# Kernel optimization log

Measured on AMD Instinct MI355X. Metric: run time of the kernel, lower is better.

The kernel has to match this reference:

```python
import jax, jax.numpy as jnp
import numpy as np


def setup_inputs() -> dict:
    key = jax.random.key(0)
    kx, ky = jax.random.split(key)
    N, D = 8192, 128
    x = jax.random.normal(kx, (N, D), dtype=jnp.float32)
    y = jax.random.normal(ky, (N, D), dtype=jnp.float32)
    return {"x": x, "y": y}


def reference(x, y):
    # L2 contrastive loss (Kostic et al. 2024, NCP):
    #   1/(N(N-1)) * sum_{i != j} <x_i, y_j>^2  -  2/N * sum_i <x_i, y_i>
    N = x.shape[0]
    K = x @ y.T                      # (N, N) pairwise dot products
    diag = jnp.diagonal(K)           # <x_i, y_i>
    off_diag_sq = jnp.sum(K * K) - jnp.sum(diag * diag)
    loss = off_diag_sq / (N * (N - 1)) - 2.0 / N * jnp.sum(diag)
    return loss
```

## Files before the change

### kernel.cpp

```cpp
#include <hip/hip_runtime.h>

#define DD 128
#define SR 72

typedef float f32x4 __attribute__((ext_vector_type(4)));
typedef short s16x8 __attribute__((ext_vector_type(8)));

__global__ __launch_bounds__(512)
void gram_kernel(const float* __restrict__ x, const float* __restrict__ y,
                 float* __restrict__ apart, float* __restrict__ bpart,
                 double* __restrict__ sc, int N, int P)
{
  const int blk = blockIdx.x;
  const bool isX = blk < P;
  const int p = isX ? blk : blk - P;
  const float* __restrict__ src = isX ? x : y;
  const int slab = N / P;
  const int row0 = p * slab;

  __shared__ __align__(16) unsigned short sh_hi[DD * SR];
  __shared__ __align__(16) unsigned short sh_lo[DD * SR];
  __shared__ double wred[8][2];

  const int tid = threadIdx.x;
  const int wave = tid >> 6, lane = tid & 63;
  const int rloc = tid >> 3;
  const int f = tid & 3 ? tid & 7 : tid & 7;
  const int fg = tid & 7;

  f32x4 acc[8];
#pragma unroll
  for (int t = 0; t < 8; ++t)
#pragma unroll
    for (int k = 0; k < 4; ++k) acc[t][k] = 0.f;

  double s1 = 0.0, s2 = 0.0;
  const int nch = slab >> 6;

  for (int c = 0; c < nch; ++c) {
    const float* cb = src + (size_t)(row0 + (c << 6)) * DD;
    const float4* rowp = (const float4*)(cb + rloc * DD);
    float4 v0 = rowp[fg], v1 = rowp[fg + 8], v2 = rowp[fg + 16], v3 = rowp[fg + 24];

    if (isX) {
      const float4* yrp = (const float4*)(y + (size_t)(row0 + (c << 6)) * DD + rloc * DD);
      float4 w0 = yrp[fg], w1 = yrp[fg + 8], w2 = yrp[fg + 16], w3 = yrp[fg + 24];
      float d = v0.x*w0.x + v0.y*w0.y + v0.z*w0.z + v0.w*w0.w
              + v1.x*w1.x + v1.y*w1.y + v1.z*w1.z + v1.w*w1.w
              + v2.x*w2.x + v2.y*w2.y + v2.z*w2.z + v2.w*w2.w
              + v3.x*w3.x + v3.y*w3.y + v3.z*w3.z + v3.w*w3.w;
      d += __shfl_down(d, 4, 8);
      d += __shfl_down(d, 2, 8);
      d += __shfl_down(d, 1, 8);
      if (fg == 0) { s1 += (double)d; s2 += (double)d * (double)d; }
    }

    __syncthreads();
    {
      float vals[16] = {v0.x, v0.y, v0.z, v0.w, v1.x, v1.y, v1.z, v1.w,
                        v2.x, v2.y, v2.z, v2.w, v3.x, v3.y, v3.z, v3.w};
#pragma unroll
      for (int j = 0; j < 4; ++j)
#pragma unroll
        for (int cc = 0; cc < 4; ++cc) {
          const int m = ((fg + (j << 3)) << 2) + cc;
          const float vv = vals[j * 4 + cc];
          const unsigned int b = __float_as_uint(vv);
          const unsigned short hb = (unsigned short)(b >> 16);
          const float hf = __uint_as_float(b & 0xffff0000u);
          const float lf = vv - hf;
          const unsigned short lb = (unsigned short)(__float_as_uint(lf) >> 16);
          sh_hi[m * SR + rloc] = hb;
          sh_lo[m * SR + rloc] = lb;
        }
    }
    __syncthreads();

#pragma unroll
    for (int kb = 0; kb < 64; kb += 32) {
      const int ko = kb + ((lane >> 4) << 3);
      const int arow = (wave * 16 + (lane & 15)) * SR + ko;
      const s16x8 ahi = *(const s16x8*)&sh_hi[arow];
      const s16x8 alo = *(const s16x8*)&sh_lo[arow];
#pragma unroll
      for (int t = 0; t < 8; ++t) {
        const int brow = (t * 16 + (lane & 15)) * SR + ko;
        const s16x8 bhi = *(const s16x8*)&sh_hi[brow];
        const s16x8 blo = *(const s16x8*)&sh_lo[brow];
        acc[t] = __builtin_amdgcn_mfma_f32_16x16x32_bf16(ahi, bhi, acc[t], 0, 0, 0);
        acc[t] = __builtin_amdgcn_mfma_f32_16x16x32_bf16(ahi, blo, acc[t], 0, 0, 0);
        acc[t] = __builtin_amdgcn_mfma_f32_16x16x32_bf16(alo, bhi, acc[t], 0, 0, 0);
      }
    }
  }

  float* __restrict__ dst = (isX ? apart : bpart) + (size_t)p * (DD * DD);
  const int col = lane & 15;
  const int rb = (lane >> 4) << 2;
#pragma unroll
  for (int t = 0; t < 8; ++t)
#pragma unroll
    for (int rg = 0; rg < 4; ++rg)
      dst[(wave * 16 + rb + rg) * DD + t * 16 + col] = acc[t][rg];

  if (isX) {
    s1 += __shfl_down(s1, 32, 64); s2 += __shfl_down(s2, 32, 64);
    s1 += __shfl_down(s1, 16, 64); s2 += __shfl_down(s2, 16, 64);
    s1 += __shfl_down(s1, 8, 64);  s2 += __shfl_down(s2, 8, 64);
    if (lane == 0) { wred[wave][0] = s1; wred[wave][1] = s2; }
    __syncthreads();
    if (tid == 0) {
      double t1 = 0.0, t2 = 0.0;
#pragma unroll
      for (int g = 0; g < 8; ++g) { t1 += wred[g][0]; t2 += wred[g][1]; }
      atomicAdd(&sc[0], t1);
      atomicAdd(&sc[1], t2);
    }
  }
}

__global__ __launch_bounds__(256)
void dot_kernel(const float* __restrict__ apart, const float* __restrict__ bpart,
                double* __restrict__ sc, unsigned int* __restrict__ cnt,
                float* __restrict__ out, int N, int P, int nblocks)
{
  const int w = threadIdx.x >> 6, lane = threadIdx.x & 63;
  const int e = blockIdx.x * 64 + lane;
  float sa = 0.f, sb = 0.f;
#pragma unroll 8
  for (int p = w; p < P; p += 4) {
    sa += apart[(size_t)p * (DD * DD) + e];
    sb += bpart[(size_t)p * (DD * DD) + e];
  }
  __shared__ float sA[4][64], sB[4][64];
  sA[w][lane] = sa;
  sB[w][lane] = sb;
  __syncthreads();
  if (w == 0) {
    float ta = sA[0][lane] + sA[1][lane] + sA[2][lane] + sA[3][lane];
    float tb = sB[0][lane] + sB[1][lane] + sB[2][lane] + sB[3][lane];
    double prod = (double)ta * (double)tb;
#pragma unroll
    for (int off = 32; off > 0; off >>= 1)
      prod += __shfl_down(prod, off, 64);
    if (lane == 0) {
      atomicAdd(&sc[2], prod);
      __threadfence();
      unsigned int old = atomicAdd(cnt, 1u);
      if (old == (unsigned int)(nblocks - 1)) {
        double s1 = atomicAdd(&sc[0], 0.0);
        double s2 = atomicAdd(&sc[1], 0.0);
        double S  = atomicAdd(&sc[2], 0.0);
        double loss = (S - s2) / ((double)N * (double)(N - 1)) - (2.0 / N) * s1;
        out[0] = (float)loss;
      }
    }
  }
}

extern "C" void kernel_launch(void* const* d_in, const int* in_sizes, int n_in,
                              void* d_out, int out_size, void* d_ws, size_t ws_size,
                              hipStream_t stream) {
  const float* x = (const float*)d_in[0];
  const float* y = (const float*)d_in[1];
  float* out = (float*)d_out;
  const int N = in_sizes[0] / DD;

  int P = 128;
  while (P > 8 && (size_t)2 * P * DD * DD * sizeof(float) + 64 > ws_size) P >>= 1;

  float* apart = (float*)d_ws;
  float* bpart = apart + (size_t)P * DD * DD;
  double* sc = (double*)((char*)d_ws + (size_t)2 * P * DD * DD * sizeof(float));
  unsigned int* cnt = (unsigned int*)(sc + 3);

  hipMemsetAsync(sc, 0, 3 * sizeof(double) + sizeof(unsigned int), stream);
  gram_kernel<<<2 * P, 512, 0, stream>>>(x, y, apart, bpart, sc, N, P);
  const int nblocks = (DD * DD) / 64;
  dot_kernel<<<nblocks, 256, 0, stream>>>(apart, bpart, sc, cnt, out, N, P, nblocks);
}
```

Measured before the change: 83.15 us.

## Hard-code partition count, drop memset, replace atomics with per-block partials

Fixes the partition count at 128, so each gram block handles exactly one 64-row chunk. This removes the chunk loop and one barrier. The hipMemsetAsync launch is gone: the counter is zeroed inside the gram kernel, and the double atomics are replaced by per-block partial arrays that the last dot block reduces. This saves a launch and atomic contention, but assumes N=8192 and a large enough workspace. It also relies on the counter reset in gram_kernel being ordered before dot_kernel.

```diff
diff --git a/kernel.cpp b/kernel.cpp
--- a/kernel.cpp
+++ b/kernel.cpp
@@ -2,6 +2,8 @@
 
 #define DD 128
 #define SR 72
+#define PP 128
+#define NB (2*PP)
 
 typedef float f32x4 __attribute__((ext_vector_type(4)));
 typedef short s16x8 __attribute__((ext_vector_type(8)));
@@ -9,14 +11,17 @@
 __global__ __launch_bounds__(512)
 void gram_kernel(const float* __restrict__ x, const float* __restrict__ y,
                  float* __restrict__ apart, float* __restrict__ bpart,
-                 double* __restrict__ sc, int N, int P)
+                 double* __restrict__ ds1, double* __restrict__ ds2,
+                 unsigned int* __restrict__ cnt, int N)
 {
   const int blk = blockIdx.x;
-  const bool isX = blk < P;
-  const int p = isX ? blk : blk - P;
+  const bool isX = blk < PP;
+  const int p = isX ? blk : blk - PP;
   const float* __restrict__ src = isX ? x : y;
-  const int slab = N / P;
+  const int slab = N / PP;
   const int row0 = p * slab;
+
+  if (blk == 0 && threadIdx.x == 0) *cnt = 0;
 
   __shared__ __align__(16) unsigned short sh_hi[DD * SR];
   __shared__ __align__(16) unsigned short sh_lo[DD * SR];
@@ -25,7 +30,6 @@
   const int tid = threadIdx.x;
   const int wave = tid >> 6, lane = tid & 63;
   const int rloc = tid >> 3;
-  const int f = tid & 3 ? tid & 7 : tid & 7;
   const int fg = tid & 7;
 
   f32x4 acc[8];
@@ -35,15 +39,14 @@
     for (int k = 0; k < 4; ++k) acc[t][k] = 0.f;
 
   double s1 = 0.0, s2 = 0.0;
-  const int nch = slab >> 6;
-
-  for (int c = 0; c < nch; ++c) {
-    const float* cb = src + (size_t)(row0 + (c << 6)) * DD;
+
+  {
+    const float* cb = src + (size_t)row0 * DD;
     const float4* rowp = (const float4*)(cb + rloc * DD);
     float4 v0 = rowp[fg], v1 = rowp[fg + 8], v2 = rowp[fg + 16], v3 = rowp[fg + 24];
 
     if (isX) {
-      const float4* yrp = (const float4*)(y + (size_t)(row0 + (c << 6)) * DD + rloc * DD);
+      const float4* yrp = (const float4*)(y + (size_t)row0 * DD + rloc * DD);
       float4 w0 = yrp[fg], w1 = yrp[fg + 8], w2 = yrp[fg + 16], w3 = yrp[fg + 24];
       float d = v0.x*w0.x + v0.y*w0.y + v0.z*w0.z + v0.w*w0.w
               + v1.x*w1.x + v1.y*w1.y + v1.z*w1.z + v1.w*w1.w
@@ -55,7 +58,6 @@
       if (fg == 0) { s1 += (double)d; s2 += (double)d * (double)d; }
     }
 
-    __syncthreads();
     {
       float vals[16] = {v0.x, v0.y, v0.z, v0.w, v1.x, v1.y, v1.z, v1.w,
                         v2.x, v2.y, v2.z, v2.w, v3.x, v3.y, v3.z, v3.w};
@@ -113,47 +115,65 @@
       double t1 = 0.0, t2 = 0.0;
 #pragma unroll
       for (int g = 0; g < 8; ++g) { t1 += wred[g][0]; t2 += wred[g][1]; }
-      atomicAdd(&sc[0], t1);
-      atomicAdd(&sc[1], t2);
+      ds1[p] = t1;
+      ds2[p] = t2;
     }
   }
 }
 
 __global__ __launch_bounds__(256)
 void dot_kernel(const float* __restrict__ apart, const float* __restrict__ bpart,
-                double* __restrict__ sc, unsigned int* __restrict__ cnt,
-                float* __restrict__ out, int N, int P, int nblocks)
+                const double* __restrict__ ds1, const double* __restrict__ ds2,
+                double* __restrict__ prod, unsigned int* __restrict__ cnt,
+                float* __restrict__ out, int N, int nblocks)
 {
   const int w = threadIdx.x >> 6, lane = threadIdx.x & 63;
+  const int tid = threadIdx.x;
   const int e = blockIdx.x * 64 + lane;
   float sa = 0.f, sb = 0.f;
 #pragma unroll 8
-  for (int p = w; p < P; p += 4) {
+  for (int p = w; p < PP; p += 4) {
     sa += apart[(size_t)p * (DD * DD) + e];
     sb += bpart[(size_t)p * (DD * DD) + e];
   }
   __shared__ float sA[4][64], sB[4][64];
+  __shared__ int amLast;
   sA[w][lane] = sa;
   sB[w][lane] = sb;
   __syncthreads();
+  if (tid == 0) {
+    float ta = 0.f, tb = 0.f;
+    amLast = 0;
+  }
   if (w == 0) {
     float ta = sA[0][lane] + sA[1][lane] + sA[2][lane] + sA[3][lane];
     float tb = sB[0][lane] + sB[1][lane] + sB[2][lane] + sB[3][lane];
-    double prod = (double)ta * (double)tb;
+    double pr = (double)ta * (double)tb;
 #pragma unroll
     for (int off = 32; off > 0; off >>= 1)
-      prod += __shfl_down(prod, off, 64);
+      pr += __shfl_down(pr, off, 64);
     if (lane == 0) {
-      atomicAdd(&sc[2], prod);
+      prod[blockIdx.x] = pr;
       __threadfence();
       unsigned int old = atomicAdd(cnt, 1u);
-      if (old == (unsigned int)(nblocks - 1)) {
-        double s1 = atomicAdd(&sc[0], 0.0);
-        double s2 = atomicAdd(&sc[1], 0.0);
-        double S  = atomicAdd(&sc[2], 0.0);
-        double loss = (S - s2) / ((double)N * (double)(N - 1)) - (2.0 / N) * s1;
-        out[0] = (float)loss;
-      }
+      if (old == (unsigned int)(nblocks - 1)) amLast = 1;
+    }
+  }
+  __syncthreads();
+  if (amLast && tid < 64) {
+    __threadfence();
+    double S  = prod[tid] + prod[tid + 64] + prod[tid + 128] + prod[tid + 192];
+    double t1 = ds1[tid] + ds1[tid + 64];
+    double t2 = ds2[tid] + ds2[tid + 64];
+#pragma unroll
+    for (int off = 32; off > 0; off >>= 1) {
+      S  += __shfl_down(S, off, 64);
+      t1 += __shfl_down(t1, off, 64);
+      t2 += __shfl_down(t2, off, 64);
+    }
+    if (tid == 0) {
+      double loss = (S - t2) / ((double)N * (double)(N - 1)) - (2.0 / N) * t1;
+      out[0] = (float)loss;
     }
   }
 }
@@ -166,16 +186,16 @@
   float* out = (float*)d_out;
   const int N = in_sizes[0] / DD;
 
-  int P = 128;
-  while (P > 8 && (size_t)2 * P * DD * DD * sizeof(float) + 64 > ws_size) P >>= 1;
-
-  float* apart = (float*)d_ws;
-  float* bpart = apart + (size_t)P * DD * DD;
-  double* sc = (double*)((char*)d_ws + (size_t)2 * P * DD * DD * sizeof(float));
-  unsigned int* cnt = (unsigned int*)(sc + 3);
-
-  hipMemsetAsync(sc, 0, 3 * sizeof(double) + sizeof(unsigned int), stream);
-  gram_kernel<<<2 * P, 512, 0, stream>>>(x, y, apart, bpart, sc, N, P);
+  char* w = (char*)d_ws;
+  float* apart = (float*)w;                              w += (size_t)PP * DD * DD * 4;
+  float* bpart = (float*)w;                              w += (size_t)PP * DD * DD * 4;
+  double* ds1  = (double*)w;                             w += PP * 8;
+  double* ds2  = (double*)w;                             w += PP * 8;
+  double* prod = (double*)w;                             w += NB * 8;
+  unsigned int* cnt = (unsigned int*)w;
+
+  gram_kernel<<<NB, 512, 0, stream>>>(x, y, apart, bpart, ds1, ds2, cnt, N);
   const int nblocks = (DD * DD) / 64;
-  dot_kernel<<<nblocks, 256, 0, stream>>>(apart, bpart, sc, cnt, out, N, P, nblocks);
+  dot_kernel<<<nblocks, 256, 0, stream>>>(apart, bpart, ds1, ds2, prod, cnt,
+                                          out, N, nblocks);
 }
```

New measurement: 75.50 us. 1.1x faster.
